# Optimization experiments

Measured on AMD Instinct MI355X. Metric: run time of the kernel, lower is better.

## Reference

```python
import jax, jax.numpy as jnp
import numpy as np
import math

B, S, D, H = 2, 1024, 4096, 32
HD = D // H  # 128
THETA = 500000.0


def setup_inputs() -> dict:
    key = jax.random.key(0)
    ks = jax.random.split(key, 6)
    x = jax.random.normal(ks[0], (B, S, D), dtype=jnp.float32)
    # RoPE frequencies (complex freqs_cis split into cos/sin), [S, HD//2]
    inv_freq = 1.0 / (THETA ** (jnp.arange(0, HD, 2, dtype=jnp.float32) / HD))
    angles = jnp.arange(S, dtype=jnp.float32)[:, None] * inv_freq[None, :]
    freqs_cos = jnp.cos(angles)
    freqs_sin = jnp.sin(angles)
    # Causal mask [1,1,S,S]: 0 on/below diag, large negative above
    neg = jnp.full((S, S), -1e9, dtype=jnp.float32)
    mask = jnp.triu(neg, k=1)[None, None]
    cache_k = jnp.zeros((B, S, H, HD), dtype=jnp.float32)
    cache_v = jnp.zeros((B, S, H, HD), dtype=jnp.float32)
    sc = 0.02
    wq = jax.random.normal(ks[1], (D, D), dtype=jnp.float32) * sc
    wk = jax.random.normal(ks[2], (D, D), dtype=jnp.float32) * sc
    wv = jax.random.normal(ks[3], (D, D), dtype=jnp.float32) * sc
    wo = jax.random.normal(ks[4], (D, D), dtype=jnp.float32) * sc
    return {"x": x, "freqs_cos": freqs_cos, "freqs_sin": freqs_sin,
            "mask": mask, "cache_k": cache_k, "cache_v": cache_v,
            "wq": wq, "wk": wk, "wv": wv, "wo": wo, "start_pos": 0}


def _apply_rope(t, cos, sin):
    # t: [B,S,H,HD]; cos/sin: [S,HD//2] -> complex multiply on (even, odd) pairs
    b, s, h, hd = t.shape
    tr = t.reshape(b, s, h, hd // 2, 2)
    te, to = tr[..., 0], tr[..., 1]
    c = cos[None, :, None, :]
    sn = sin[None, :, None, :]
    oe = te * c - to * sn
    oo = te * sn + to * c
    return jnp.stack([oe, oo], axis=-1).reshape(b, s, h, hd)


def reference(x, freqs_cos, freqs_sin, mask, cache_k, cache_v, wq, wk, wv, wo, start_pos):
    bsz, seqlen, dim = x.shape
    xq = (x @ wq.T).reshape(bsz, seqlen, H, HD)
    xk = (x @ wk.T).reshape(bsz, seqlen, H, HD)
    xv = (x @ wv.T).reshape(bsz, seqlen, H, HD)
    xq = _apply_rope(xq, freqs_cos, freqs_sin)
    xk = _apply_rope(xk, freqs_cos, freqs_sin)
    # KV-cache update
    cache_k = jax.lax.dynamic_update_slice(cache_k, xk, (0, start_pos, 0, 0))
    cache_v = jax.lax.dynamic_update_slice(cache_v, xv, (0, start_pos, 0, 0))
    keys = cache_k[:bsz, : start_pos + seqlen]    # [B,K,H,HD]
    values = cache_v[:bsz, : start_pos + seqlen]
    scores = jnp.einsum("bqhd,bkhd->bhqk", xq, keys) / math.sqrt(HD)
    scores = scores + mask
    probs = jax.nn.softmax(scores.astype(jnp.float32), axis=-1).astype(xq.dtype)
    out = jnp.einsum("bhqk,bkhd->bqhd", probs, values).reshape(bsz, seqlen, dim)
    return out @ wo.T
```

## Files before the change

kernel.cpp:

```cpp
#include <hip/hip_runtime.h>
#include <cstdint>
#include <cstddef>

typedef __bf16 bf16;
typedef bf16  bf16x8  __attribute__((ext_vector_type(8)));
typedef bf16  bf16x4  __attribute__((ext_vector_type(4)));
typedef float floatx4 __attribute__((ext_vector_type(4)));

#define D_MODEL 4096
#define NROWS   2048
#define SEQ     1024
#define NHEADS  32
#define HDIM    128

__device__ __forceinline__ void async16(const void* g, void* s) {
    __builtin_amdgcn_global_load_lds(
        (__attribute__((address_space(1))) void*)g,
        (__attribute__((address_space(3))) void*)s,
        16, 0, 0);
}

__global__ __launch_bounds__(256) void cvt_kernel(const float* __restrict__ in,
                                                  bf16* __restrict__ out, int n4) {
    int i = blockIdx.x * 256 + threadIdx.x;
    if (i >= n4) return;
    const float4 v = ((const float4*)in)[i];
    bf16x4 o;
    o[0] = (bf16)v.x; o[1] = (bf16)v.y; o[2] = (bf16)v.z; o[3] = (bf16)v.w;
    ((bf16x4*)out)[i] = o;
}

template<bool F32OUT, bool ROPE>
__global__ __launch_bounds__(256) void gemm_bt(const bf16* __restrict__ A,
                                               const bf16* __restrict__ B0,
                                               void* __restrict__ C0,
                                               const float* __restrict__ fc,
                                               const float* __restrict__ fs) {
    __shared__ __align__(16) bf16 As[128 * 32];
    __shared__ __align__(16) bf16 Bs[128 * 32];
    const int tid  = threadIdx.x;
    const int lane = tid & 63;
    const int wave = tid >> 6;
    const int col  = lane & 15;
    const int quad = lane >> 4;
    const int bm = blockIdx.x * 128;
    const int bn = blockIdx.y * 128;
    const int wm = (wave >> 1) * 64;
    const int wn = (wave & 1) * 64;
    const bf16* Bw = B0 + (size_t)blockIdx.z * ((size_t)D_MODEL * D_MODEL);

    floatx4 acc[4][4] = {};

    int srow[2], sg[2];
#pragma unroll
    for (int j = 0; j < 2; j++) {
        int c = j * 256 + tid;
        srow[j] = c >> 2;
        sg[j]   = (c & 3) ^ ((srow[j] >> 1) & 3);
    }

    for (int k0 = 0; k0 < D_MODEL; k0 += 32) {
#pragma unroll
        for (int j = 0; j < 2; j++) {
            void* dstA = (void*)(As + (size_t)(j * 256 + wave * 64) * 8);
            void* dstB = (void*)(Bs + (size_t)(j * 256 + wave * 64) * 8);
            async16(A  + (size_t)(bm + srow[j]) * D_MODEL + k0 + sg[j] * 8, dstA);
            async16(Bw + (size_t)(bn + srow[j]) * D_MODEL + k0 + sg[j] * 8, dstB);
        }
        __syncthreads();
        bf16x8 a[4], b[4];
#pragma unroll
        for (int i = 0; i < 4; i++) {
            int r = wm + i * 16 + col;
            a[i] = *(const bf16x8*)&As[r * 32 + (quad ^ ((r >> 1) & 3)) * 8];
        }
#pragma unroll
        for (int j = 0; j < 4; j++) {
            int r = wn + j * 16 + col;
            b[j] = *(const bf16x8*)&Bs[r * 32 + (quad ^ ((r >> 1) & 3)) * 8];
        }
#pragma unroll
        for (int i = 0; i < 4; i++)
#pragma unroll
            for (int j = 0; j < 4; j++)
                acc[i][j] = __builtin_amdgcn_mfma_f32_16x16x32_bf16(a[i], b[j], acc[i][j], 0, 0, 0);
        __syncthreads();
    }

    const float qs = (ROPE && blockIdx.z == 0) ? 0.08838834764831845f : 1.0f;
    const bool do_rope = ROPE && (blockIdx.z <= 1);

#pragma unroll
    for (int i = 0; i < 4; i++) {
#pragma unroll
        for (int j = 0; j < 4; j++) {
            int row = bm + wm + i * 16 + quad * 4;
            int cg  = bn + wn + j * 16 + col;
#pragma unroll
            for (int r = 0; r < 4; r++) {
                float v = acc[i][j][r];
                if (do_rope) {
                    float pv = __shfl_xor(v, 1);
                    int s = (row + r) & 1023;
                    int d = (cg & 127) >> 1;
                    float c  = fc[s * 64 + d] * qs;
                    float sn = fs[s * 64 + d] * qs;
                    v = v * c + pv * ((cg & 1) ? sn : -sn);
                }
                if constexpr (F32OUT) {
                    ((float*)C0)[(size_t)(row + r) * D_MODEL + cg] = v;
                } else {
                    bf16* C = (bf16*)C0 + (size_t)blockIdx.z * ((size_t)NROWS * D_MODEL);
                    C[(size_t)(row + r) * D_MODEL + cg] = (bf16)v;
                }
            }
        }
    }
}

#define PST 72

__global__ __launch_bounds__(256, 2) void attn_kernel(const bf16* __restrict__ Qb,
                                                      const bf16* __restrict__ Kb,
                                                      const bf16* __restrict__ Vb,
                                                      bf16* __restrict__ Ob) {
    __shared__ __align__(16) bf16 Ks[64 * 128];
    __shared__ __align__(16) bf16 Vt[128 * 64];
    __shared__ __align__(16) bf16 Ps[4 * 32 * PST];

    const int tid  = threadIdx.x;
    const int lane = tid & 63;
    const int wave = tid >> 6;
    const int col  = lane & 15;
    const int quad = lane >> 4;
    const int hb   = tid & 15;
    const int kb   = tid >> 4;

    const int b   = blockIdx.z;
    const int h   = blockIdx.y;
    const int q0b = blockIdx.x * 128;
    const int q0w = q0b + wave * 32;
    const size_t bh = (size_t)(b * SEQ) * D_MODEL + h * HDIM;

    bf16x8 qf[2][4];
#pragma unroll
    for (int qi = 0; qi < 2; qi++)
#pragma unroll
        for (int kc = 0; kc < 4; kc++)
            qf[qi][kc] = *(const bf16x8*)(Qb + bh + (size_t)(q0w + qi * 16 + col) * D_MODEL + kc * 32 + quad * 8);

    floatx4 o[2][8];
    floatx4 ol[2];
#pragma unroll
    for (int qi = 0; qi < 2; qi++) {
        ol[qi] = (floatx4){0.f, 0.f, 0.f, 0.f};
#pragma unroll
        for (int c = 0; c < 8; c++) o[qi][c] = (floatx4){0.f, 0.f, 0.f, 0.f};
    }

    bf16x8 ones;
#pragma unroll
    for (int t = 0; t < 8; t++) ones[t] = (bf16)1.0f;

    bf16* Psw = Ps + wave * 32 * PST;
    const int nkt = blockIdx.x * 2 + 2;

    for (int kt = 0; kt < nkt; kt++) {
        const int key0 = kt * 64;
#pragma unroll
        for (int it = 0; it < 4; it++) {
            int l = it * 256 + tid;
            int row = l >> 4, p = l & 15;
            int g = (p & 8) | ((p ^ (row & 7) ^ ((row >> 3) & 7)) & 7);
            async16(Kb + bh + (size_t)(key0 + row) * D_MODEL + g * 8,
                    (void*)(Ks + (size_t)(it * 256 + wave * 64) * 8));
        }
        {
            uint32_t uv[4][4];
#pragma unroll
            for (int i = 0; i < 4; i++) {
                uint4 t = *(const uint4*)(Vb + bh + (size_t)(key0 + kb * 4 + i) * D_MODEL + hb * 8);
                uv[i][0] = t.x; uv[i][1] = t.y; uv[i][2] = t.z; uv[i][3] = t.w;
            }
#pragma unroll
            for (int j = 0; j < 8; j++) {
                uint32_t sel = (j & 1) ? 0x07060302u : 0x05040100u;
                uint32_t w0 = __builtin_amdgcn_perm(uv[1][j >> 1], uv[0][j >> 1], sel);
                uint32_t w1 = __builtin_amdgcn_perm(uv[3][j >> 1], uv[2][j >> 1], sel);
                int row = hb * 8 + j;
                int p = ((kb >> 1) ^ (row & 7) ^ ((row >> 3) & 7)) & 7;
                uint2* dst = (uint2*)&Vt[row * 64 + p * 8 + (kb & 1) * 4];
                *dst = (uint2){w0, w1};
            }
        }
        __syncthreads();

        if (key0 <= q0w + 31) {
            const bool masked = (key0 + 63 > q0w);
            floatx4 sf[2][4];
#pragma unroll
            for (int qi = 0; qi < 2; qi++)
#pragma unroll
                for (int f = 0; f < 4; f++) sf[qi][f] = (floatx4){0.f, 0.f, 0.f, 0.f};
#pragma unroll
            for (int kc = 0; kc < 4; kc++)
#pragma unroll
                for (int f = 0; f < 4; f++) {
                    int row = f * 16 + col;
                    int g = kc * 4 + quad;
                    int p = (g & 8) | ((g ^ (row & 7) ^ ((row >> 3) & 7)) & 7);
                    bf16x8 kf = *(const bf16x8*)&Ks[row * 128 + p * 8];
                    sf[0][f] = __builtin_amdgcn_mfma_f32_16x16x32_bf16(qf[0][kc], kf, sf[0][f], 0, 0, 0);
                    sf[1][f] = __builtin_amdgcn_mfma_f32_16x16x32_bf16(qf[1][kc], kf, sf[1][f], 0, 0, 0);
                }
#pragma unroll
            for (int qi = 0; qi < 2; qi++)
#pragma unroll
                for (int f = 0; f < 4; f++) {
                    int key = key0 + f * 16 + col;
#pragma unroll
                    for (int r = 0; r < 4; r++) {
                        float pv;
                        if (masked)
                            pv = (key <= q0w + qi * 16 + quad * 4 + r) ? __expf(sf[qi][f][r]) : 0.f;
                        else
                            pv = __expf(sf[qi][f][r]);
                        Psw[(qi * 16 + quad * 4 + r) * PST + f * 16 + col] = (bf16)pv;
                    }
                }
#pragma unroll
            for (int kc = 0; kc < 2; kc++) {
                bf16x8 pa0 = *(const bf16x8*)&Psw[(0 * 16 + col) * PST + kc * 32 + quad * 8];
                bf16x8 pa1 = *(const bf16x8*)&Psw[(1 * 16 + col) * PST + kc * 32 + quad * 8];
                ol[0] = __builtin_amdgcn_mfma_f32_16x16x32_bf16(pa0, ones, ol[0], 0, 0, 0);
                ol[1] = __builtin_amdgcn_mfma_f32_16x16x32_bf16(pa1, ones, ol[1], 0, 0, 0);
#pragma unroll
                for (int c = 0; c < 8; c++) {
                    int row = c * 16 + col;
                    int g = kc * 4 + quad;
                    int p = (g ^ (row & 7) ^ ((row >> 3) & 7)) & 7;
                    bf16x8 vf = *(const bf16x8*)&Vt[row * 64 + p * 8];
                    o[0][c] = __builtin_amdgcn_mfma_f32_16x16x32_bf16(pa0, vf, o[0][c], 0, 0, 0);
                    o[1][c] = __builtin_amdgcn_mfma_f32_16x16x32_bf16(pa1, vf, o[1][c], 0, 0, 0);
                }
            }
        }
        __syncthreads();
    }

#pragma unroll
    for (int qi = 0; qi < 2; qi++) {
        float inv[4];
#pragma unroll
        for (int r = 0; r < 4; r++) inv[r] = 1.0f / ol[qi][r];
#pragma unroll
        for (int c = 0; c < 8; c++)
#pragma unroll
            for (int r = 0; r < 4; r++)
                Ob[bh + (size_t)(q0w + qi * 16 + quad * 4 + r) * D_MODEL + c * 16 + col] =
                    (bf16)(o[qi][c][r] * inv[r]);
    }
}

extern "C" void kernel_launch(void* const* d_in, const int* in_sizes, int n_in,
                              void* d_out, int out_size, void* d_ws, size_t ws_size,
                              hipStream_t stream) {
    const float* x  = (const float*)d_in[0];
    const float* fc = (const float*)d_in[1];
    const float* fs = (const float*)d_in[2];
    const float* wq = (const float*)d_in[6];
    const float* wk = (const float*)d_in[7];
    const float* wv = (const float*)d_in[8];
    const float* wo = (const float*)d_in[9];

    char* ws    = (char*)d_ws;
    bf16* xb    = (bf16*)(ws);
    bf16* wb    = (bf16*)(ws + 16777216ull);
    bf16* qkvb  = (bf16*)(ws + 117440512ull);
    bf16* attnb = (bf16*)(ws + 167772160ull);

    cvt_kernel<<<8192,  256, 0, stream>>>(x,  xb,                   2097152);
    cvt_kernel<<<16384, 256, 0, stream>>>(wq, wb + 0ull * 16777216, 4194304);
    cvt_kernel<<<16384, 256, 0, stream>>>(wk, wb + 1ull * 16777216, 4194304);
    cvt_kernel<<<16384, 256, 0, stream>>>(wv, wb + 2ull * 16777216, 4194304);

    gemm_bt<false, true><<<dim3(16, 32, 3), 256, 0, stream>>>(xb, wb, (void*)qkvb, fc, fs);

    cvt_kernel<<<16384, 256, 0, stream>>>(wo, wb, 4194304);

    attn_kernel<<<dim3(8, 32, 2), 256, 0, stream>>>(qkvb, qkvb + 8388608ull,
                                                    qkvb + 16777216ull, attnb);

    gemm_bt<true, false><<<dim3(16, 32, 1), 256, 0, stream>>>(attnb, wb, d_out, nullptr, nullptr);
}
```

Before: 809.6 us.

## Split RoPE into standalone kernel, drop LDS swizzle, reverse attention block order

Moves the RoPE rotation and query scaling out of the QKV GEMM epilogue into a separate vectorized elementwise kernel operating on bf16 Q/K. It also removes the XOR swizzle from the GEMM shared-memory tile addressing and reverses the query-block order for the second batch in attention to balance causal work. The separate RoPE pass adds an extra read/write of Q and K and rounds to bf16 before rotation. Removing the swizzle may introduce LDS bank conflicts in the GEMM inner loop.

```diff
diff --git a/kernel.cpp b/kernel.cpp
--- a/kernel.cpp
+++ b/kernel.cpp
@@ -30,12 +30,40 @@
     ((bf16x4*)out)[i] = o;
 }
 
-template<bool F32OUT, bool ROPE>
+__global__ __launch_bounds__(256) void rope_kernel(bf16* __restrict__ Qb,
+                                                   bf16* __restrict__ Kb,
+                                                   const float* __restrict__ fc,
+                                                   const float* __restrict__ fs) {
+    int t = blockIdx.x * 256 + threadIdx.x;
+    const bool isK = (t >> 20) != 0;
+    bf16* p = isK ? Kb : Qb;
+    const float qs = isK ? 1.0f : 0.08838834764831845f;
+    int i = t & 1048575;
+    int e = i * 8;
+    int row = e >> 12;
+    int coff = e & 4095;
+    int s = row & 1023;
+    int d0 = (coff & 127) >> 1;
+
+    bf16x8 v = *(bf16x8*)(p + (size_t)row * D_MODEL + coff);
+    float4 c4 = *(const float4*)&fc[s * 64 + d0];
+    float4 s4 = *(const float4*)&fs[s * 64 + d0];
+    float cc[4] = {c4.x, c4.y, c4.z, c4.w};
+    float ss[4] = {s4.x, s4.y, s4.z, s4.w};
+    bf16x8 o;
+#pragma unroll
+    for (int j = 0; j < 4; j++) {
+        float e0 = (float)v[2 * j], e1 = (float)v[2 * j + 1];
+        o[2 * j]     = (bf16)((e0 * cc[j] - e1 * ss[j]) * qs);
+        o[2 * j + 1] = (bf16)((e0 * ss[j] + e1 * cc[j]) * qs);
+    }
+    *(bf16x8*)(p + (size_t)row * D_MODEL + coff) = o;
+}
+
+template<bool F32OUT>
 __global__ __launch_bounds__(256) void gemm_bt(const bf16* __restrict__ A,
                                                const bf16* __restrict__ B0,
-                                               void* __restrict__ C0,
-                                               const float* __restrict__ fc,
-                                               const float* __restrict__ fs) {
+                                               void* __restrict__ C0) {
     __shared__ __align__(16) bf16 As[128 * 32];
     __shared__ __align__(16) bf16 Bs[128 * 32];
     const int tid  = threadIdx.x;
@@ -51,34 +79,25 @@
 
     floatx4 acc[4][4] = {};
 
-    int srow[2], sg[2];
-#pragma unroll
-    for (int j = 0; j < 2; j++) {
-        int c = j * 256 + tid;
-        srow[j] = c >> 2;
-        sg[j]   = (c & 3) ^ ((srow[j] >> 1) & 3);
-    }
-
     for (int k0 = 0; k0 < D_MODEL; k0 += 32) {
 #pragma unroll
         for (int j = 0; j < 2; j++) {
+            int c   = j * 256 + tid;
+            int row = c >> 2;
+            int kc  = (c & 3) * 8;
             void* dstA = (void*)(As + (size_t)(j * 256 + wave * 64) * 8);
             void* dstB = (void*)(Bs + (size_t)(j * 256 + wave * 64) * 8);
-            async16(A  + (size_t)(bm + srow[j]) * D_MODEL + k0 + sg[j] * 8, dstA);
-            async16(Bw + (size_t)(bn + srow[j]) * D_MODEL + k0 + sg[j] * 8, dstB);
+            async16(A  + (size_t)(bm + row) * D_MODEL + k0 + kc, dstA);
+            async16(Bw + (size_t)(bn + row) * D_MODEL + k0 + kc, dstB);
         }
         __syncthreads();
         bf16x8 a[4], b[4];
 #pragma unroll
-        for (int i = 0; i < 4; i++) {
-            int r = wm + i * 16 + col;
-            a[i] = *(const bf16x8*)&As[r * 32 + (quad ^ ((r >> 1) & 3)) * 8];
-        }
-#pragma unroll
-        for (int j = 0; j < 4; j++) {
-            int r = wn + j * 16 + col;
-            b[j] = *(const bf16x8*)&Bs[r * 32 + (quad ^ ((r >> 1) & 3)) * 8];
-        }
+        for (int i = 0; i < 4; i++)
+            a[i] = *(const bf16x8*)&As[(wm + i * 16 + col) * 32 + quad * 8];
+#pragma unroll
+        for (int j = 0; j < 4; j++)
+            b[j] = *(const bf16x8*)&Bs[(wn + j * 16 + col) * 32 + quad * 8];
 #pragma unroll
         for (int i = 0; i < 4; i++)
 #pragma unroll
@@ -87,9 +106,6 @@
         __syncthreads();
     }
 
-    const float qs = (ROPE && blockIdx.z == 0) ? 0.08838834764831845f : 1.0f;
-    const bool do_rope = ROPE && (blockIdx.z <= 1);
-
 #pragma unroll
     for (int i = 0; i < 4; i++) {
 #pragma unroll
@@ -98,20 +114,11 @@
             int cg  = bn + wn + j * 16 + col;
 #pragma unroll
             for (int r = 0; r < 4; r++) {
-                float v = acc[i][j][r];
-                if (do_rope) {
-                    float pv = __shfl_xor(v, 1);
-                    int s = (row + r) & 1023;
-                    int d = (cg & 127) >> 1;
-                    float c  = fc[s * 64 + d] * qs;
-                    float sn = fs[s * 64 + d] * qs;
-                    v = v * c + pv * ((cg & 1) ? sn : -sn);
-                }
                 if constexpr (F32OUT) {
-                    ((float*)C0)[(size_t)(row + r) * D_MODEL + cg] = v;
+                    ((float*)C0)[(size_t)(row + r) * D_MODEL + cg] = acc[i][j][r];
                 } else {
                     bf16* C = (bf16*)C0 + (size_t)blockIdx.z * ((size_t)NROWS * D_MODEL);
-                    C[(size_t)(row + r) * D_MODEL + cg] = (bf16)v;
+                    C[(size_t)(row + r) * D_MODEL + cg] = (bf16)acc[i][j][r];
                 }
             }
         }
@@ -138,7 +145,8 @@
 
     const int b   = blockIdx.z;
     const int h   = blockIdx.y;
-    const int q0b = blockIdx.x * 128;
+    const int ex  = b ? (7 - blockIdx.x) : blockIdx.x;
+    const int q0b = ex * 128;
     const int q0w = q0b + wave * 32;
     const size_t bh = (size_t)(b * SEQ) * D_MODEL + h * HDIM;
 
@@ -163,7 +171,7 @@
     for (int t = 0; t < 8; t++) ones[t] = (bf16)1.0f;
 
     bf16* Psw = Ps + wave * 32 * PST;
-    const int nkt = blockIdx.x * 2 + 2;
+    const int nkt = ex * 2 + 2;
 
     for (int kt = 0; kt < nkt; kt++) {
         const int key0 = kt * 64;
@@ -284,12 +292,14 @@
     cvt_kernel<<<16384, 256, 0, stream>>>(wk, wb + 1ull * 16777216, 4194304);
     cvt_kernel<<<16384, 256, 0, stream>>>(wv, wb + 2ull * 16777216, 4194304);
 
-    gemm_bt<false, true><<<dim3(16, 32, 3), 256, 0, stream>>>(xb, wb, (void*)qkvb, fc, fs);
+    gemm_bt<false><<<dim3(16, 32, 3), 256, 0, stream>>>(xb, wb, (void*)qkvb);
 
     cvt_kernel<<<16384, 256, 0, stream>>>(wo, wb, 4194304);
+
+    rope_kernel<<<8192, 256, 0, stream>>>(qkvb, qkvb + 8388608ull, fc, fs);
 
     attn_kernel<<<dim3(8, 32, 2), 256, 0, stream>>>(qkvb, qkvb + 8388608ull,
                                                     qkvb + 16777216ull, attnb);
 
-    gemm_bt<true, false><<<dim3(16, 32, 1), 256, 0, stream>>>(attnb, wb, d_out, nullptr, nullptr);
-}
+    gemm_bt<true><<<dim3(16, 32, 1), 256, 0, stream>>>(attnb, wb, d_out);
+}
```

Result: faster. 724.7 us (-10.5%).
